# Kernel tuning notes

Measured on AMD Instinct MI355X. Metric: run time of the kernel, lower is better.

The kernel has to match this reference:

```python
import jax, jax.numpy as jnp
import numpy as np
from jax import lax

B, H, W = 16, 400, 400
NUM_PALETTE = 16

def _conv(x, w, b, stride, pad):
    y = lax.conv_general_dilated(x, w, (stride, stride), [(pad, pad), (pad, pad)],
                                 dimension_numbers=('NCHW', 'OIHW', 'NCHW'))
    return y + b[None, :, None, None]

def _leaky(x):
    return jnp.where(x >= 0, x, 0.01 * x)

def _palette(x, w1, b1, w2, b2, w3, b3, w4, b4, w5, b5, w6, b6):
    h = _leaky(_conv(x, w1, b1, 2, 1))   # [B,6,200,200]
    h = _leaky(_conv(h, w2, b2, 2, 1))   # [B,12,100,100]
    h = _leaky(_conv(h, w3, b3, 2, 1))   # [B,12,50,50]
    h = _leaky(_conv(h, w4, b4, 2, 1))   # [B,12,25,25]
    h = _leaky(_conv(h, w5, b5, 2, 1))   # [B,6,13,13]
    h = jax.nn.relu(_conv(h, w6, b6, 1, 0))  # [B,3,13,13]
    return h

def setup_inputs() -> dict:
    key = jax.random.key(0)
    ks = jax.random.split(key, 14)
    def he(k, shape):
        fan_in = shape[1] * shape[2] * shape[3]
        return jax.random.normal(k, shape, jnp.float32) * np.float32(np.sqrt(2.0 / fan_in))
    return {
        'x': jax.random.normal(ks[0], (B, 3, H, W), jnp.float32),
        'b_logits': jax.random.normal(ks[1], (B, NUM_PALETTE, H, W), jnp.float32),
        'w1': he(ks[2], (6, 3, 3, 3)),   'b1': jnp.zeros((6,), jnp.float32),
        'w2': he(ks[3], (12, 6, 3, 3)),  'b2': jnp.zeros((12,), jnp.float32),
        'w3': he(ks[4], (12, 12, 3, 3)), 'b3': jnp.zeros((12,), jnp.float32),
        'w4': he(ks[5], (12, 12, 3, 3)), 'b4': jnp.zeros((12,), jnp.float32),
        'w5': he(ks[6], (6, 12, 3, 3)),  'b5': jnp.zeros((6,), jnp.float32),
        'w6': he(ks[7], (3, 6, 1, 1)),   'b6': jnp.zeros((3,), jnp.float32),
    }

def reference(x, b_logits, w1, b1, w2, b2, w3, b3, w4, b4, w5, b5, w6, b6):
    # palette branch -> [B,3,13,13]; top-left 4x4 holds the 16 palette colors
    c = _palette(x, w1, b1, w2, b2, w3, b3, w4, b4, w5, b5, w6, b6)
    pal = c[:, :, :4, :4].reshape(c.shape[0], 3, NUM_PALETTE)  # [B,3,16], k = row*4+col
    # softmax over palette classes, one-hot of argmax via max-equality (ties kept, as in torch)
    probs = jax.nn.softmax(b_logits, axis=1)                    # [B,16,H,W]
    mx = jnp.max(probs, axis=1, keepdims=True)
    onehot = (probs == mx).astype(x.dtype)                      # [B,16,H,W]
    # per-pixel palette gather expressed as a contraction over the 16 classes
    result = jnp.einsum('bkhw,bck->bchw', onehot, pal)          # [B,3,H,W]
    return result
```

## Files before the change

kernel.cpp:

```cpp
#include <hip/hip_runtime.h>

#define HW 160000
#define WIMG 400

__global__ __launch_bounds__(256) void conv1_k(const float* __restrict__ x,
                                               const float* __restrict__ w,
                                               const float* __restrict__ bias,
                                               float* __restrict__ out) {
  int idx = blockIdx.x * 256 + threadIdx.x;
  int j = idx & 63;
  int i = (idx >> 6) & 63;
  int t = idx >> 12;
  int o = t % 6;
  int b = t / 6;
  float acc = bias[o];
#pragma unroll
  for (int c = 0; c < 3; c++) {
    const float* xc = x + (size_t)(b * 3 + c) * HW;
    const float* wc = w + (o * 3 + c) * 9;
#pragma unroll
    for (int di = 0; di < 3; di++) {
      int xi = 2 * i - 1 + di;
      if (xi < 0) continue;
#pragma unroll
      for (int dj = 0; dj < 3; dj++) {
        int xj = 2 * j - 1 + dj;
        if (xj < 0) continue;
        acc = fmaf(xc[xi * WIMG + xj], wc[di * 3 + dj], acc);
      }
    }
  }
  out[idx] = acc >= 0.f ? acc : 0.01f * acc;
}

template <int N, int CIN>
__global__ __launch_bounds__(256) void convs_k(const float* __restrict__ in,
                                               const float* __restrict__ w,
                                               const float* __restrict__ bias,
                                               float* __restrict__ out,
                                               int cout) {
  int idx = blockIdx.x * 256 + threadIdx.x;
  int j = idx & (N - 1);
  int i = (idx / N) & (N - 1);
  int t = idx / (N * N);
  int o = t % cout;
  int b = t / cout;
  float acc = bias[o];
#pragma unroll
  for (int c = 0; c < CIN; c++) {
    const float* xc = in + (size_t)(b * CIN + c) * (4 * N * N);
    const float* wc = w + (o * CIN + c) * 9;
#pragma unroll
    for (int di = 0; di < 3; di++) {
      int xi = 2 * i - 1 + di;
      if (xi < 0) continue;
#pragma unroll
      for (int dj = 0; dj < 3; dj++) {
        int xj = 2 * j - 1 + dj;
        if (xj < 0) continue;
        acc = fmaf(xc[xi * 2 * N + xj], wc[di * 3 + dj], acc);
      }
    }
  }
  out[idx] = acc >= 0.f ? acc : 0.01f * acc;
}

__global__ __launch_bounds__(256) void conv6_k(const float* __restrict__ c5,
                                               const float* __restrict__ w,
                                               const float* __restrict__ bias,
                                               float* __restrict__ pal) {
  int idx = blockIdx.x * 256 + threadIdx.x;
  int k = idx & 15;
  int t = idx >> 4;
  int o = t % 3;
  int b = t / 3;
  float a = bias[o];
#pragma unroll
  for (int c = 0; c < 6; c++) a = fmaf(c5[b * 96 + c * 16 + k], w[o * 6 + c], a);
  pal[b * 48 + o * 16 + k] = a > 0.f ? a : 0.f;
}

__global__ __launch_bounds__(256) void gather_k(const float* __restrict__ logits,
                                                const float* __restrict__ pal,
                                                float* __restrict__ out) {
  __shared__ float ps[48];
  int b = blockIdx.y;
  int tid = threadIdx.x;
  if (tid < 48) ps[tid] = pal[b * 48 + tid];
  __syncthreads();
  int q = blockIdx.x * 256 + tid;
  if (q >= HW / 4) return;
  const float* lg = logits + (size_t)b * 16 * HW + q * 4;

  float4 v = *(const float4*)(lg);
  float mx[4] = {v.x, v.y, v.z, v.w};
  float p0 = ps[0], p1 = ps[16], p2 = ps[32];
  float r0[4] = {p0, p0, p0, p0};
  float r1[4] = {p1, p1, p1, p1};
  float r2[4] = {p2, p2, p2, p2};

#pragma unroll
  for (int k = 1; k < 16; k++) {
    float4 t = *(const float4*)(lg + (size_t)k * HW);
    float q0 = ps[k], q1 = ps[16 + k], q2 = ps[32 + k];
    float vv[4] = {t.x, t.y, t.z, t.w};
#pragma unroll
    for (int pp = 0; pp < 4; pp++) {
      float val = vv[pp];
      bool gt = val > mx[pp];
      bool ge = val >= mx[pp];
      mx[pp] = ge ? val : mx[pp];
      r0[pp] = (gt ? 0.f : r0[pp]) + (ge ? q0 : 0.f);
      r1[pp] = (gt ? 0.f : r1[pp]) + (ge ? q1 : 0.f);
      r2[pp] = (gt ? 0.f : r2[pp]) + (ge ? q2 : 0.f);
    }
  }
  float* ob = out + (size_t)b * 3 * HW + q * 4;
  *(float4*)(ob) = make_float4(r0[0], r0[1], r0[2], r0[3]);
  *(float4*)(ob + HW) = make_float4(r1[0], r1[1], r1[2], r1[3]);
  *(float4*)(ob + 2 * HW) = make_float4(r2[0], r2[1], r2[2], r2[3]);
}

extern "C" void kernel_launch(void* const* d_in, const int* in_sizes, int n_in,
                              void* d_out, int out_size, void* d_ws, size_t ws_size,
                              hipStream_t stream) {
  const float* x    = (const float*)d_in[0];
  const float* blog = (const float*)d_in[1];
  const float* w1 = (const float*)d_in[2];
  const float* b1 = (const float*)d_in[3];
  const float* w2 = (const float*)d_in[4];
  const float* b2 = (const float*)d_in[5];
  const float* w3 = (const float*)d_in[6];
  const float* b3 = (const float*)d_in[7];
  const float* w4 = (const float*)d_in[8];
  const float* b4 = (const float*)d_in[9];
  const float* w5 = (const float*)d_in[10];
  const float* b5 = (const float*)d_in[11];
  const float* w6 = (const float*)d_in[12];
  const float* b6 = (const float*)d_in[13];
  float* out = (float*)d_out;

  float* c1  = (float*)d_ws;
  float* c2  = c1 + 16 * 6 * 64 * 64;
  float* c3  = c2 + 16 * 12 * 32 * 32;
  float* c4  = c3 + 16 * 12 * 16 * 16;
  float* c5  = c4 + 16 * 12 * 8 * 8;
  float* pal = c5 + 16 * 6 * 4 * 4;

  conv1_k<<<1536, 256, 0, stream>>>(x, w1, b1, c1);
  convs_k<32, 6><<<768, 256, 0, stream>>>(c1, w2, b2, c2, 12);
  convs_k<16, 12><<<192, 256, 0, stream>>>(c2, w3, b3, c3, 12);
  convs_k<8, 12><<<48, 256, 0, stream>>>(c3, w4, b4, c4, 12);
  convs_k<4, 12><<<6, 256, 0, stream>>>(c4, w5, b5, c5, 6);
  conv6_k<<<3, 256, 0, stream>>>(c5, w6, b6, pal);
  gather_k<<<dim3((HW / 4 + 255) / 256, 16), 256, 0, stream>>>(blog, pal, out);
}
```

Measured before the change: 336.6 us.

## Fuse conv3-conv6 into one per-batch kernel and prefetch all logits in gather

Merges the small conv3, conv4, conv5 and conv6 launches into a single kernel, one block per batch, that keeps intermediates in shared memory. This removes three kernel launches and the global round-trips between those tiny stages. In exchange, only 16 blocks run that serial chain. Separately, the gather kernel now issues all 16 logit float4 loads up front to raise memory-level parallelism, at the cost of more registers.

Measured after the change: 383.9 us. 1.14x slower.

```diff
diff --git a/kernel.cpp b/kernel.cpp
--- a/kernel.cpp
+++ b/kernel.cpp
@@ -33,23 +33,21 @@
   out[idx] = acc >= 0.f ? acc : 0.01f * acc;
 }
 
-template <int N, int CIN>
-__global__ __launch_bounds__(256) void convs_k(const float* __restrict__ in,
+__global__ __launch_bounds__(256) void conv2_k(const float* __restrict__ in,
                                                const float* __restrict__ w,
                                                const float* __restrict__ bias,
-                                               float* __restrict__ out,
-                                               int cout) {
+                                               float* __restrict__ out) {
   int idx = blockIdx.x * 256 + threadIdx.x;
-  int j = idx & (N - 1);
-  int i = (idx / N) & (N - 1);
-  int t = idx / (N * N);
-  int o = t % cout;
-  int b = t / cout;
+  int j = idx & 31;
+  int i = (idx >> 5) & 31;
+  int t = idx >> 10;
+  int o = t % 12;
+  int b = t / 12;
   float acc = bias[o];
 #pragma unroll
-  for (int c = 0; c < CIN; c++) {
-    const float* xc = in + (size_t)(b * CIN + c) * (4 * N * N);
-    const float* wc = w + (o * CIN + c) * 9;
+  for (int c = 0; c < 6; c++) {
+    const float* xc = in + (size_t)(b * 6 + c) * 4096;
+    const float* wc = w + (o * 6 + c) * 9;
 #pragma unroll
     for (int di = 0; di < 3; di++) {
       int xi = 2 * i - 1 + di;
@@ -58,26 +56,105 @@
       for (int dj = 0; dj < 3; dj++) {
         int xj = 2 * j - 1 + dj;
         if (xj < 0) continue;
-        acc = fmaf(xc[xi * 2 * N + xj], wc[di * 3 + dj], acc);
+        acc = fmaf(xc[xi * 64 + xj], wc[di * 3 + dj], acc);
       }
     }
   }
   out[idx] = acc >= 0.f ? acc : 0.01f * acc;
 }
 
-__global__ __launch_bounds__(256) void conv6_k(const float* __restrict__ c5,
-                                               const float* __restrict__ w,
-                                               const float* __restrict__ bias,
-                                               float* __restrict__ pal) {
-  int idx = blockIdx.x * 256 + threadIdx.x;
-  int k = idx & 15;
-  int t = idx >> 4;
-  int o = t % 3;
-  int b = t / 3;
-  float a = bias[o];
-#pragma unroll
-  for (int c = 0; c < 6; c++) a = fmaf(c5[b * 96 + c * 16 + k], w[o * 6 + c], a);
-  pal[b * 48 + o * 16 + k] = a > 0.f ? a : 0.f;
+__global__ __launch_bounds__(256) void conv3456_k(
+    const float* __restrict__ c2, const float* __restrict__ w3,
+    const float* __restrict__ b3, const float* __restrict__ w4,
+    const float* __restrict__ b4, const float* __restrict__ w5,
+    const float* __restrict__ b5, const float* __restrict__ w6,
+    const float* __restrict__ b6, float* __restrict__ pal) {
+  __shared__ float s[12288];
+  __shared__ float o3[3072];
+  int tid = threadIdx.x;
+  int b = blockIdx.x;
+
+  for (int t = tid; t < 12288; t += 256) s[t] = c2[(size_t)b * 12288 + t];
+  __syncthreads();
+
+#pragma unroll
+  for (int r = 0; r < 12; r++) {
+    int idx = tid + 256 * r;
+    int j = idx & 15, i = (idx >> 4) & 15, o = idx >> 8;
+    float a = b3[o];
+    for (int c = 0; c < 12; c++) {
+      const float* wc = w3 + (o * 12 + c) * 9;
+      const float* sc = s + c * 1024;
+#pragma unroll
+      for (int di = 0; di < 3; di++) {
+        int xi = 2 * i - 1 + di;
+        if (xi < 0) continue;
+#pragma unroll
+        for (int dj = 0; dj < 3; dj++) {
+          int xj = 2 * j - 1 + dj;
+          if (xj < 0) continue;
+          a = fmaf(sc[xi * 32 + xj], wc[di * 3 + dj], a);
+        }
+      }
+    }
+    o3[idx] = a >= 0.f ? a : 0.01f * a;
+  }
+  __syncthreads();
+
+#pragma unroll
+  for (int r = 0; r < 3; r++) {
+    int idx = tid + 256 * r;
+    int j = idx & 7, i = (idx >> 3) & 7, o = idx >> 6;
+    float a = b4[o];
+    for (int c = 0; c < 12; c++) {
+      const float* wc = w4 + (o * 12 + c) * 9;
+      const float* sc = o3 + c * 256;
+#pragma unroll
+      for (int di = 0; di < 3; di++) {
+        int xi = 2 * i - 1 + di;
+        if (xi < 0) continue;
+#pragma unroll
+        for (int dj = 0; dj < 3; dj++) {
+          int xj = 2 * j - 1 + dj;
+          if (xj < 0) continue;
+          a = fmaf(sc[xi * 16 + xj], wc[di * 3 + dj], a);
+        }
+      }
+    }
+    __syncthreads();
+    s[idx] = a >= 0.f ? a : 0.01f * a;
+  }
+  __syncthreads();
+
+  if (tid < 96) {
+    int j = tid & 3, i = (tid >> 2) & 3, o = tid >> 4;
+    float a = b5[o];
+    for (int c = 0; c < 12; c++) {
+      const float* wc = w5 + (o * 12 + c) * 9;
+      const float* sc = s + c * 64;
+#pragma unroll
+      for (int di = 0; di < 3; di++) {
+        int xi = 2 * i - 1 + di;
+        if (xi < 0) continue;
+#pragma unroll
+        for (int dj = 0; dj < 3; dj++) {
+          int xj = 2 * j - 1 + dj;
+          if (xj < 0) continue;
+          a = fmaf(sc[xi * 8 + xj], wc[di * 3 + dj], a);
+        }
+      }
+    }
+    s[1024 + tid] = a >= 0.f ? a : 0.01f * a;
+  }
+  __syncthreads();
+
+  if (tid < 48) {
+    int k = tid & 15, o = tid >> 4;
+    float a = b6[o];
+#pragma unroll
+    for (int c = 0; c < 6; c++) a = fmaf(s[1024 + c * 16 + k], w6[o * 6 + c], a);
+    pal[b * 48 + o * 16 + k] = a > 0.f ? a : 0.f;
+  }
 }
 
 __global__ __launch_bounds__(256) void gather_k(const float* __restrict__ logits,
@@ -92,8 +169,11 @@
   if (q >= HW / 4) return;
   const float* lg = logits + (size_t)b * 16 * HW + q * 4;
 
-  float4 v = *(const float4*)(lg);
-  float mx[4] = {v.x, v.y, v.z, v.w};
+  float4 t[16];
+#pragma unroll
+  for (int k = 0; k < 16; k++) t[k] = *(const float4*)(lg + (size_t)k * HW);
+
+  float mx[4] = {t[0].x, t[0].y, t[0].z, t[0].w};
   float p0 = ps[0], p1 = ps[16], p2 = ps[32];
   float r0[4] = {p0, p0, p0, p0};
   float r1[4] = {p1, p1, p1, p1};
@@ -101,9 +181,8 @@
 
 #pragma unroll
   for (int k = 1; k < 16; k++) {
-    float4 t = *(const float4*)(lg + (size_t)k * HW);
     float q0 = ps[k], q1 = ps[16 + k], q2 = ps[32 + k];
-    float vv[4] = {t.x, t.y, t.z, t.w};
+    float vv[4] = {t[k].x, t[k].y, t[k].z, t[k].w};
 #pragma unroll
     for (int pp = 0; pp < 4; pp++) {
       float val = vv[pp];
@@ -142,16 +221,10 @@
 
   float* c1  = (float*)d_ws;
   float* c2  = c1 + 16 * 6 * 64 * 64;
-  float* c3  = c2 + 16 * 12 * 32 * 32;
-  float* c4  = c3 + 16 * 12 * 16 * 16;
-  float* c5  = c4 + 16 * 12 * 8 * 8;
-  float* pal = c5 + 16 * 6 * 4 * 4;
+  float* pal = c2 + 16 * 12 * 32 * 32;
 
   conv1_k<<<1536, 256, 0, stream>>>(x, w1, b1, c1);
-  convs_k<32, 6><<<768, 256, 0, stream>>>(c1, w2, b2, c2, 12);
-  convs_k<16, 12><<<192, 256, 0, stream>>>(c2, w3, b3, c3, 12);
-  convs_k<8, 12><<<48, 256, 0, stream>>>(c3, w4, b4, c4, 12);
-  convs_k<4, 12><<<6, 256, 0, stream>>>(c4, w5, b5, c5, 6);
-  conv6_k<<<3, 256, 0, stream>>>(c5, w6, b6, pal);
+  conv2_k<<<768, 256, 0, stream>>>(c1, w2, b2, c2);
+  conv3456_k<<<16, 256, 0, stream>>>(c2, w3, b3, w4, b4, w5, b5, w6, b6, pal);
   gather_k<<<dim3((HW / 4 + 255) / 256, 16), 256, 0, stream>>>(blog, pal, out);
 }
```
